# Kernel optimization log

Hardware: AMD Instinct MI355X
Metric: run time of the kernel (lower is better)

Reference implementation:

```python
import jax, jax.numpy as jnp
import numpy as np

N = 100000   # nodes
E = 1600000  # edges (avg degree 16)
IN, H, OUT = 64, 128, 1


def setup_inputs() -> dict:
    key = jax.random.key(0)
    ks = jax.random.split(key, 12)
    s = 0.05
    return {
        "x": jax.random.normal(ks[0], (N, IN), jnp.float32),
        "edge_index": jax.random.randint(ks[1], (2, E), 0, N, dtype=jnp.int64),
        "Wl1": jax.random.normal(ks[2], (IN, H), jnp.float32) * s,
        "Wr1": jax.random.normal(ks[3], (IN, H), jnp.float32) * s,
        "b1": jnp.zeros((H,), jnp.float32),
        "ln_g": jnp.ones((H,), jnp.float32),
        "ln_b": jnp.zeros((H,), jnp.float32),
        "Wres": jax.random.normal(ks[4], (IN, H), jnp.float32) * s,
        "bres": jnp.zeros((H,), jnp.float32),
        "Wl2": jax.random.normal(ks[5], (H, H), jnp.float32) * s,
        "Wr2": jax.random.normal(ks[6], (H, H), jnp.float32) * s,
        "b2": jnp.zeros((H,), jnp.float32),
        "Wl3": jax.random.normal(ks[7], (H, H), jnp.float32) * s,
        "Wr3": jax.random.normal(ks[8], (H, H), jnp.float32) * s,
        "b3": jnp.zeros((H,), jnp.float32),
        "Wl4": jax.random.normal(ks[9], (H, OUT), jnp.float32) * s,
        "Wr4": jax.random.normal(ks[10], (H, OUT), jnp.float32) * s,
        "b4": jnp.zeros((OUT,), jnp.float32),
    }


def _sage(h, src, dst, deg_inv, Wl, Wr, b):
    # PyG SAGEConv, aggr='mean': lin_l(mean_{j in N(i)} h_j) + lin_r(h_i)
    agg = jax.ops.segment_sum(h[src], dst, num_segments=N) * deg_inv[:, None]
    return agg @ Wl + h @ Wr + b


def _layernorm(h, g, b, eps=1e-5):
    mu = jnp.mean(h, axis=-1, keepdims=True)
    var = jnp.mean((h - mu) ** 2, axis=-1, keepdims=True)
    return (h - mu) * jax.lax.rsqrt(var + eps) * g + b


def reference(x, edge_index, Wl1, Wr1, b1, ln_g, ln_b, Wres, bres,
              Wl2, Wr2, b2, Wl3, Wr3, b3, Wl4, Wr4, b4):
    src, dst = edge_index[0], edge_index[1]
    deg = jax.ops.segment_sum(jnp.ones((E,), jnp.float32), dst, num_segments=N)
    deg_inv = 1.0 / jnp.maximum(deg, 1.0)

    h = jax.nn.relu(_layernorm(_sage(x, src, dst, deg_inv, Wl1, Wr1, b1), ln_g, ln_b))
    h = h + x @ Wres + bres              # residual (in_channel != hidden_channel)
    h = jax.nn.relu(_sage(h, src, dst, deg_inv, Wl2, Wr2, b2))   # dropout: eval no-op
    h = jax.nn.relu(_sage(h, src, dst, deg_inv, Wl3, Wr3, b3))
    out = _sage(h, src, dst, deg_inv, Wl4, Wr4, b4)
    return out.squeeze(-1)
```

## Files before the change

### kernel.cpp

```cpp
#include <hip/hip_runtime.h>
#include <hip/hip_bf16.h>

#define N_NODES 100000
#define N_EDGES 1600000

#define NBKT 782
#define SCAT_BLOCKS 240
#define BKT_CHUNK 6667

#define SORT_BLOCKS 40
#define SORT_CHUNK 2500
#define BH2_N (NBKT * SCAT_BLOCKS)
#define BHB ((BH2_N + 1023) / 1024)
#define XBF_BLOCKS 6250

#define NSTRIPS 6250
#define GEMM_BLOCKS 782

typedef __attribute__((ext_vector_type(8))) short short8v;
typedef __attribute__((ext_vector_type(4))) float float4v;

__device__ __forceinline__ unsigned short f2bf(float f) {
    unsigned int u = __float_as_uint(f);
    u = (u + 0x7FFFu + ((u >> 16) & 1u)) >> 16;
    return (unsigned short)u;
}
__device__ __forceinline__ float bf2f(unsigned short b) {
    return __uint_as_float((unsigned int)b << 16);
}

typedef __attribute__((address_space(1))) const unsigned int gld_g_t;
typedef __attribute__((address_space(3))) unsigned int gld_l_t;
__device__ __forceinline__ void gld_lds16(const void* g, void* l) {
    __builtin_amdgcn_global_load_lds((gld_g_t*)g, (gld_l_t*)l, 16, 0, 0);
}

#define SWZ128(row, ksh) ((row) * 128 + ((ksh) ^ (((row) & 7) << 3)))
#define SWZ256(row, ksh) ((row) * 256 + ((ksh) ^ (((row) & 7) << 3)))

__global__ __launch_bounds__(256) void hist_xbf_kernel(const int* __restrict__ ei, int* __restrict__ bh2,
                                                       const float* __restrict__ x, unsigned short* __restrict__ xsrc) {
    __shared__ int h[NBKT];
    int tid = threadIdx.x;
    if (blockIdx.x < SCAT_BLOCKS) {
        for (int i = tid; i < NBKT; i += 256) h[i] = 0;
        __syncthreads();
        int start = blockIdx.x * BKT_CHUNK;
        int end = start + BKT_CHUNK; if (end > N_EDGES) end = N_EDGES;
        for (int i = start + tid; i < end; i += 256) {
            int d = ei[N_EDGES + i];
            atomicAdd(&h[d >> 7], 1);
        }
        __syncthreads();
        for (int i = tid; i < NBKT; i += 256) bh2[i * SCAT_BLOCKS + blockIdx.x] = h[i];
    } else {
        int idx = (blockIdx.x - SCAT_BLOCKS) * 256 + tid;
        if (idx < N_NODES * 16) {
            int node = idx >> 4;
            int f0 = (idx & 15) * 4;
            float4 v = *(const float4*)(x + (size_t)idx * 4);
            ushort4 o;
            o.x = f2bf(v.x); o.y = f2bf(v.y); o.z = f2bf(v.z); o.w = f2bf(v.w);
            *(ushort4*)(xsrc + (size_t)node * 64 + f0) = o;
        }
    }
}

__global__ __launch_bounds__(256) void gscan_a_kernel(const int* __restrict__ in, int* __restrict__ bsum, int n) {
    __shared__ int lds[256];
    int tid = threadIdx.x;
    int base = blockIdx.x * 1024 + tid * 4;
    int s = 0;
    #pragma unroll
    for (int i = 0; i < 4; i++) s += (base + i < n) ? in[base + i] : 0;
    lds[tid] = s;
    __syncthreads();
    for (int off = 128; off; off >>= 1) {
        if (tid < off) lds[tid] += lds[tid + off];
        __syncthreads();
    }
    if (tid == 0) bsum[blockIdx.x] = lds[0];
}

__global__ __launch_bounds__(256) void gscan_c_kernel(int* __restrict__ data, const int* __restrict__ bsum,
                                                      int nb, int n) {
    __shared__ int sb[256];
    __shared__ int lds[256];
    int tid = threadIdx.x;
    sb[tid] = (tid < nb) ? bsum[tid] : 0;
    __syncthreads();
    for (int off = 1; off < 256; off <<= 1) {
        int y = 0;
        if (tid >= off) y = sb[tid - off];
        __syncthreads();
        if (tid >= off) sb[tid] += y;
        __syncthreads();
    }
    int blockbase = (blockIdx.x == 0) ? 0 : sb[blockIdx.x - 1];

    int base = blockIdx.x * 1024 + tid * 4;
    int v[4];
    int s = 0;
    #pragma unroll
    for (int i = 0; i < 4; i++) {
        v[i] = (base + i < n) ? data[base + i] : 0;
        s += v[i];
    }
    lds[tid] = s;
    __syncthreads();
    for (int off = 1; off < 256; off <<= 1) {
        int y = 0;
        if (tid >= off) y = lds[tid - off];
        __syncthreads();
        if (tid >= off) lds[tid] += y;
        __syncthreads();
    }
    int run = blockbase + lds[tid] - s;
    #pragma unroll
    for (int i = 0; i < 4; i++) {
        if (base + i < n) data[base + i] = run;
        run += v[i];
    }
}

__global__ __launch_bounds__(256) void bkt_scatter2_kernel(const int* __restrict__ ei, const int* __restrict__ bh2,
                                                           int* __restrict__ packed) {
    __shared__ int h[NBKT];
    __shared__ int base[NBKT];
    int tid = threadIdx.x;
    for (int i = tid; i < NBKT; i += 256) { h[i] = 0; base[i] = bh2[i * SCAT_BLOCKS + blockIdx.x]; }
    __syncthreads();
    int start = blockIdx.x * BKT_CHUNK;
    int end = start + BKT_CHUNK; if (end > N_EDGES) end = N_EDGES;
    for (int i = start + tid; i < end; i += 256) {
        int s = ei[i];
        int d = ei[N_EDGES + i];
        int b = d >> 7;
        int pos = base[b] + atomicAdd(&h[b], 1);
        packed[pos] = (s << 7) | (d & 127);
    }
}

__global__ __launch_bounds__(256) void bkt_build_kernel(const int* __restrict__ packed, const int* __restrict__ bh2,
                                                        int* __restrict__ deg, int* __restrict__ row_ptr,
                                                        int* __restrict__ col) {
    __shared__ int c[128];
    __shared__ int rp[128];
    int tid = threadIdx.x;
    int s0 = bh2[blockIdx.x * SCAT_BLOCKS];
    int s1 = (blockIdx.x + 1 < NBKT) ? bh2[(blockIdx.x + 1) * SCAT_BLOCKS] : N_EDGES;
    if (tid < 128) c[tid] = 0;
    __syncthreads();
    for (int i = s0 + tid; i < s1; i += 256) atomicAdd(&c[packed[i] & 127], 1);
    __syncthreads();
    if (tid < 128) rp[tid] = c[tid];
    __syncthreads();
    for (int off = 1; off < 128; off <<= 1) {
        int y = 0;
        if (tid >= off && tid < 128) y = rp[tid - off];
        __syncthreads();
        if (tid >= off && tid < 128) rp[tid] += y;
        __syncthreads();
    }
    int node = blockIdx.x * 128 + tid;
    if (tid < 128) {
        rp[tid] = s0 + rp[tid] - c[tid];
        if (node < N_NODES) {
            deg[node] = c[tid];
            row_ptr[node] = rp[tid];
        }
        c[tid] = 0;
    }
    if (blockIdx.x == 0 && tid == 0) row_ptr[N_NODES] = N_EDGES;
    __syncthreads();
    for (int i = s0 + tid; i < s1; i += 256) {
        int p = packed[i];
        int dl = p & 127;
        int pos = rp[dl] + atomicAdd(&c[dl], 1);
        col[pos] = p >> 7;
    }
}

__global__ __launch_bounds__(256) void dsort_hist_kernel(const int* __restrict__ deg, int* __restrict__ bh) {
    __shared__ int h[64];
    int tid = threadIdx.x;
    if (tid < 64) h[tid] = 0;
    __syncthreads();
    int start = blockIdx.x * SORT_CHUNK;
    int end = start + SORT_CHUNK; if (end > N_NODES) end = N_NODES;
    for (int i = start + tid; i < end; i += 256) atomicAdd(&h[63 - min(deg[i], 63)], 1);
    __syncthreads();
    if (tid < 64) bh[tid * SORT_BLOCKS + blockIdx.x] = h[tid];
}

__global__ __launch_bounds__(256) void dsort_scat_kernel(const int* __restrict__ deg, const int* __restrict__ bh,
                                                         int* __restrict__ ord) {
    __shared__ int sbh[64 * SORT_BLOCKS];
    __shared__ int ps[256];
    __shared__ int h[64];
    int tid = threadIdx.x;
    int v[10];
    int s = 0;
    #pragma unroll
    for (int k = 0; k < 10; k++) { v[k] = bh[tid * 10 + k]; s += v[k]; }
    ps[tid] = s;
    if (tid < 64) h[tid] = 0;
    __syncthreads();
    for (int off = 1; off < 256; off <<= 1) {
        int y = 0;
        if (tid >= off) y = ps[tid - off];
        __syncthreads();
        if (tid >= off) ps[tid] += y;
        __syncthreads();
    }
    int run = ps[tid] - s;
    #pragma unroll
    for (int k = 0; k < 10; k++) { sbh[tid * 10 + k] = run; run += v[k]; }
    __syncthreads();
    int start = blockIdx.x * SORT_CHUNK;
    int end = start + SORT_CHUNK; if (end > N_NODES) end = N_NODES;
    for (int i = start + tid; i < end; i += 256) {
        int b = 63 - min(deg[i], 63);
        int pos = sbh[b * SORT_BLOCKS + blockIdx.x] + atomicAdd(&h[b], 1);
        ord[pos] = i;
    }
}

#define ACC4(u) { a0 += bf2f(u.x); a1 += bf2f(u.y); a2 += bf2f(u.z); a3 += bf2f(u.w); }

__global__ __launch_bounds__(256) void agg64_kernel(const unsigned short* __restrict__ xsrc,
                                                    unsigned short* __restrict__ aggx,
                                                    const int* __restrict__ row_ptr, const int* __restrict__ col,
                                                    const int* __restrict__ ord) {
    int tid = threadIdx.x;
    int slot = blockIdx.x * 16 + (tid >> 4);
    if (slot >= N_NODES) return;
    int i = ord[slot];
    int f0 = (tid & 15) * 4;
    int s = row_ptr[i], e = row_ptr[i + 1];
    float a0 = 0.f, a1 = 0.f, a2 = 0.f, a3 = 0.f;
    int t = s;
    while (t + 7 < e) {
        int j0 = col[t], j1 = col[t + 1], j2 = col[t + 2], j3 = col[t + 3];
        int j4 = col[t + 4], j5 = col[t + 5], j6 = col[t + 6], j7 = col[t + 7];
        ushort4 u0 = *(const ushort4*)(xsrc + (size_t)j0 * 64 + f0);
        ushort4 u1 = *(const ushort4*)(xsrc + (size_t)j1 * 64 + f0);
        ushort4 u2 = *(const ushort4*)(xsrc + (size_t)j2 * 64 + f0);
        ushort4 u3 = *(const ushort4*)(xsrc + (size_t)j3 * 64 + f0);
        ushort4 u4 = *(const ushort4*)(xsrc + (size_t)j4 * 64 + f0);
        ushort4 u5 = *(const ushort4*)(xsrc + (size_t)j5 * 64 + f0);
        ushort4 u6 = *(const ushort4*)(xsrc + (size_t)j6 * 64 + f0);
        ushort4 u7 = *(const ushort4*)(xsrc + (size_t)j7 * 64 + f0);
        ACC4(u0) ACC4(u1) ACC4(u2) ACC4(u3) ACC4(u4) ACC4(u5) ACC4(u6) ACC4(u7)
        t += 8;
    }
    if (t + 3 < e) {
        int j0 = col[t], j1 = col[t + 1], j2 = col[t + 2], j3 = col[t + 3];
        ushort4 u0 = *(const ushort4*)(xsrc + (size_t)j0 * 64 + f0);
        ushort4 u1 = *(const ushort4*)(xsrc + (size_t)j1 * 64 + f0);
        ushort4 u2 = *(const ushort4*)(xsrc + (size_t)j2 * 64 + f0);
        ushort4 u3 = *(const ushort4*)(xsrc + (size_t)j3 * 64 + f0);
        ACC4(u0) ACC4(u1) ACC4(u2) ACC4(u3)
        t += 4;
    }
    if (t + 1 < e) {
        int j0 = col[t], j1 = col[t + 1];
        ushort4 u0 = *(const ushort4*)(xsrc + (size_t)j0 * 64 + f0);
        ushort4 u1 = *(const ushort4*)(xsrc + (size_t)j1 * 64 + f0);
        ACC4(u0) ACC4(u1)
        t += 2;
    }
    if (t < e) {
        ushort4 u0 = *(const ushort4*)(xsrc + (size_t)col[t] * 64 + f0);
        ACC4(u0)
    }
    float di = 1.0f / fmaxf((float)(e - s), 1.0f);
    ushort4 o;
    o.x = f2bf(a0 * di); o.y = f2bf(a1 * di); o.z = f2bf(a2 * di); o.w = f2bf(a3 * di);
    *(ushort4*)(aggx + (size_t)i * 64 + f0) = o;
}

__global__ __launch_bounds__(256) void agg128_kernel(const unsigned short* __restrict__ hsrc,
                                                     unsigned short* __restrict__ aggh,
                                                     const int* __restrict__ row_ptr, const int* __restrict__ col,
                                                     const int* __restrict__ ord) {
    int tid = threadIdx.x;
    int slot = blockIdx.x * 8 + (tid >> 5);
    if (slot >= N_NODES) return;
    int i = ord[slot];
    int f0 = (tid & 31) * 4;
    int s = row_ptr[i], e = row_ptr[i + 1];
    float a0 = 0.f, a1 = 0.f, a2 = 0.f, a3 = 0.f;
    int t = s;
    while (t + 7 < e) {
        int j0 = col[t], j1 = col[t + 1], j2 = col[t + 2], j3 = col[t + 3];
        int j4 = col[t + 4], j5 = col[t + 5], j6 = col[t + 6], j7 = col[t + 7];
        ushort4 u0 = *(const ushort4*)(hsrc + (size_t)j0 * 128 + f0);
        ushort4 u1 = *(const ushort4*)(hsrc + (size_t)j1 * 128 + f0);
        ushort4 u2 = *(const ushort4*)(hsrc + (size_t)j2 * 128 + f0);
        ushort4 u3 = *(const ushort4*)(hsrc + (size_t)j3 * 128 + f0);
        ushort4 u4 = *(const ushort4*)(hsrc + (size_t)j4 * 128 + f0);
        ushort4 u5 = *(const ushort4*)(hsrc + (size_t)j5 * 128 + f0);
        ushort4 u6 = *(const ushort4*)(hsrc + (size_t)j6 * 128 + f0);
        ushort4 u7 = *(const ushort4*)(hsrc + (size_t)j7 * 128 + f0);
        ACC4(u0) ACC4(u1) ACC4(u2) ACC4(u3) ACC4(u4) ACC4(u5) ACC4(u6) ACC4(u7)
        t += 8;
    }
    if (t + 3 < e) {
        int j0 = col[t], j1 = col[t + 1], j2 = col[t + 2], j3 = col[t + 3];
        ushort4 u0 = *(const ushort4*)(hsrc + (size_t)j0 * 128 + f0);
        ushort4 u1 = *(const ushort4*)(hsrc + (size_t)j1 * 128 + f0);
        ushort4 u2 = *(const ushort4*)(hsrc + (size_t)j2 * 128 + f0);
        ushort4 u3 = *(const ushort4*)(hsrc + (size_t)j3 * 128 + f0);
        ACC4(u0) ACC4(u1) ACC4(u2) ACC4(u3)
        t += 4;
    }
    if (t + 1 < e) {
        int j0 = col[t], j1 = col[t + 1];
        ushort4 u0 = *(const ushort4*)(hsrc + (size_t)j0 * 128 + f0);
        ushort4 u1 = *(const ushort4*)(hsrc + (size_t)j1 * 128 + f0);
        ACC4(u0) ACC4(u1)
        t += 2;
    }
    if (t < e) {
        ushort4 u0 = *(const ushort4*)(hsrc + (size_t)col[t] * 128 + f0);
        ACC4(u0)
    }
    float di = 1.0f / fmaxf((float)(e - s), 1.0f);
    ushort4 o;
    o.x = f2bf(a0 * di); o.y = f2bf(a1 * di); o.z = f2bf(a2 * di); o.w = f2bf(a3 * di);
    *(ushort4*)(aggh + (size_t)i * 128 + f0) = o;
}

__global__ __launch_bounds__(256) void wprep_all_kernel(const float* __restrict__ Wr1, const float* __restrict__ Wl1,
                                                        const float* __restrict__ Wres,
                                                        const float* __restrict__ Wl2, const float* __restrict__ Wr2,
                                                        const float* __restrict__ Wl3, const float* __restrict__ Wr3,
                                                        unsigned short* __restrict__ Bt1,
                                                        unsigned short* __restrict__ Bt2,
                                                        unsigned short* __restrict__ Bt3) {
    int idx = blockIdx.x * 256 + threadIdx.x;
    int seg = idx >> 15;
    int loc = idx & 32767;
    if (seg == 0) {
        int n = loc >> 7;
        int k = loc & 127;
        float v;
        if (n < 128) v = (k < 64) ? Wr1[k * 128 + n] : Wl1[(k - 64) * 128 + n];
        else         v = (k < 64) ? Wres[k * 128 + (n - 128)] : 0.f;
        Bt1[loc] = f2bf(v);
    } else if (seg == 1) {
        int n = loc >> 8;
        int k = loc & 255;
        float v = (k < 128) ? Wr2[k * 128 + n] : Wl2[(k - 128) * 128 + n];
        Bt2[loc] = f2bf(v);
    } else if (seg == 2) {
        int n = loc >> 8;
        int k = loc & 255;
        float v = (k < 128) ? Wr3[k * 128 + n] : Wl3[(k - 128) * 128 + n];
        Bt3[loc] = f2bf(v);
    }
}

__global__ __launch_bounds__(512) void mgemm1_ln_kernel(const unsigned short* __restrict__ Ax,
                                                        const unsigned short* __restrict__ Aa,
                                                        const unsigned short* __restrict__ Bt,
                                                        const float* __restrict__ b1, const float* __restrict__ ln_g,
                                                        const float* __restrict__ ln_b, const float* __restrict__ bres,
                                                        unsigned short* __restrict__ hsrc) {
    __shared__ unsigned short Bs[32768];
    int tid = threadIdx.x;
    int wave = tid >> 6, lane = tid & 63;
    int lm = lane & 15, lk = (lane >> 4) * 8;

    #pragma unroll
    for (int rnd = 0; rnd < 8; rnd++) {
        int Lb = rnd * 8192 + tid * 16;
        int row = Lb >> 8;
        int sb = (Lb & 255) ^ ((row & 7) << 4);
        gld_lds16(Bt + (size_t)row * 128 + (sb >> 1), &Bs[Lb >> 1]);
    }
    __syncthreads();

    int strip = blockIdx.x * 8 + wave;
    if (strip >= NSTRIPS) return;
    int m0 = strip * 16;

    float4v accT[8], accR[8];
    #pragma unroll
    for (int j = 0; j < 8; j++) { accT[j] = (float4v)0.f; accR[j] = (float4v)0.f; }

    const unsigned short* arx = Ax + (size_t)(m0 + lm) * 64 + lk;
    const unsigned short* ara = Aa + (size_t)(m0 + lm) * 64 + lk;
    #pragma unroll
    for (int k0 = 0; k0 < 128; k0 += 32) {
        short8v af = (k0 < 64) ? *(const short8v*)(arx + k0) : *(const short8v*)(ara + (k0 - 64));
        short8v bf[8];
        #pragma unroll
        for (int j = 0; j < 8; j++)
            bf[j] = *(const short8v*)&Bs[SWZ128(j * 16 + lm, k0 + lk)];
        #pragma unroll
        for (int j = 0; j < 8; j++)
            accT[j] = __builtin_amdgcn_mfma_f32_16x16x32_bf16(af, bf[j], accT[j], 0, 0, 0);
        if (k0 < 64) {
            short8v bg[8];
            #pragma unroll
            for (int j = 0; j < 8; j++)
                bg[j] = *(const short8v*)&Bs[SWZ128(128 + j * 16 + lm, k0 + lk)];
            #pragma unroll
            for (int j = 0; j < 8; j++)
                accR[j] = __builtin_amdgcn_mfma_f32_16x16x32_bf16(af, bg[j], accR[j], 0, 0, 0);
        }
    }

    float b1v[8], gv[8], bbv[8], brv[8];
    #pragma unroll
    for (int j = 0; j < 8; j++) {
        int cc = j * 16 + lm;
        b1v[j] = b1[cc]; gv[j] = ln_g[cc]; bbv[j] = ln_b[cc]; brv[j] = bres[cc];
    }
    int q4 = lane >> 4;
    #pragma unroll
    for (int r = 0; r < 4; r++) {
        float sp = 0.f, sq = 0.f;
        #pragma unroll
        for (int j = 0; j < 8; j++) {
            float tv = accT[j][r] + b1v[j];
            sp += tv; sq += tv * tv;
        }
        #pragma unroll
        for (int off = 1; off < 16; off <<= 1) {
            sp += __shfl_xor(sp, off);
            sq += __shfl_xor(sq, off);
        }
        float mu = sp * (1.f / 128.f);
        float var = sq * (1.f / 128.f) - mu * mu;
        float rstd = rsqrtf(var + 1e-5f);
        int gm = m0 + q4 * 4 + r;
        #pragma unroll
        for (int j = 0; j < 8; j++) {
            float tv = accT[j][r] + b1v[j];
            float y = fmaxf((tv - mu) * rstd * gv[j] + bbv[j], 0.f) + accR[j][r] + brv[j];
            hsrc[(size_t)gm * 128 + j * 16 + lm] = f2bf(y);
        }
    }
}

__global__ __launch_bounds__(512) void mgemm_kernel(const unsigned short* __restrict__ Ah,
                                                    const unsigned short* __restrict__ Aa,
                                                    const unsigned short* __restrict__ Bt,
                                                    const float* __restrict__ bias,
                                                    unsigned short* __restrict__ C) {
    __shared__ unsigned short Bs[32768];
    int tid = threadIdx.x;
    int wave = tid >> 6, lane = tid & 63;
    int lm = lane & 15, lk = (lane >> 4) * 8;

    #pragma unroll
    for (int rnd = 0; rnd < 8; rnd++) {
        int Lb = rnd * 8192 + tid * 16;
        int row = Lb >> 9;
        int sb = (Lb & 511) ^ ((row & 7) << 4);
        gld_lds16(Bt + ((size_t)row << 8) + (sb >> 1), &Bs[Lb >> 1]);
    }
    __syncthreads();

    int strip = blockIdx.x * 8 + wave;
    if (strip >= NSTRIPS) return;
    int m0 = strip * 16;

    float4v acc[8];
    #pragma unroll
    for (int j = 0; j < 8; j++) acc[j] = (float4v)0.f;

    const unsigned short* arh = Ah + (size_t)(m0 + lm) * 128 + lk;
    const unsigned short* ara = Aa + (size_t)(m0 + lm) * 128 + lk;
    #pragma unroll
    for (int k0 = 0; k0 < 256; k0 += 32) {
        short8v af = (k0 < 128) ? *(const short8v*)(arh + k0) : *(const short8v*)(ara + (k0 - 128));
        short8v bf[8];
        #pragma unroll
        for (int j = 0; j < 8; j++)
            bf[j] = *(const short8v*)&Bs[SWZ256(j * 16 + lm, k0 + lk)];
        #pragma unroll
        for (int j = 0; j < 8; j++)
            acc[j] = __builtin_amdgcn_mfma_f32_16x16x32_bf16(af, bf[j], acc[j], 0, 0, 0);
    }

    int q4 = lane >> 4;
    #pragma unroll
    for (int j = 0; j < 8; j++) {
        int cc = j * 16 + lm;
        float bv = bias[cc];
        #pragma unroll
        for (int r = 0; r < 4; r++) {
            int m = m0 + q4 * 4 + r;
            C[(size_t)m * 128 + cc] = f2bf(fmaxf(acc[j][r] + bv, 0.f));
        }
    }
}

__global__ __launch_bounds__(512) void mgemm_pq_kernel(const unsigned short* __restrict__ Ah,
                                                       const unsigned short* __restrict__ Aa,
                                                       const unsigned short* __restrict__ Bt,
                                                       const float* __restrict__ bias,
                                                       const float* __restrict__ Wl4, const float* __restrict__ Wr4,
                                                       const float* __restrict__ b4,
                                                       float* __restrict__ p, float* __restrict__ q) {
    __shared__ unsigned short Bs[32768];
    int tid = threadIdx.x;
    int wave = tid >> 6, lane = tid & 63;
    int lm = lane & 15, lk = (lane >> 4) * 8;

    #pragma unroll
    for (int rnd = 0; rnd < 8; rnd++) {
        int Lb = rnd * 8192 + tid * 16;
        int row = Lb >> 9;
        int sb = (Lb & 511) ^ ((row & 7) << 4);
        gld_lds16(Bt + ((size_t)row << 8) + (sb >> 1), &Bs[Lb >> 1]);
    }
    __syncthreads();

    int strip = blockIdx.x * 8 + wave;
    if (strip >= NSTRIPS) return;
    int m0 = strip * 16;

    float4v acc[8];
    #pragma unroll
    for (int j = 0; j < 8; j++) acc[j] = (float4v)0.f;

    const unsigned short* arh = Ah + (size_t)(m0 + lm) * 128 + lk;
    const unsigned short* ara = Aa + (size_t)(m0 + lm) * 128 + lk;
    #pragma unroll
    for (int k0 = 0; k0 < 256; k0 += 32) {
        short8v af = (k0 < 128) ? *(const short8v*)(arh + k0) : *(const short8v*)(ara + (k0 - 128));
        short8v bf[8];
        #pragma unroll
        for (int j = 0; j < 8; j++)
            bf[j] = *(const short8v*)&Bs[SWZ256(j * 16 + lm, k0 + lk)];
        #pragma unroll
        for (int j = 0; j < 8; j++)
            acc[j] = __builtin_amdgcn_mfma_f32_16x16x32_bf16(af, bf[j], acc[j], 0, 0, 0);
    }

    float b3v[8], wlv[8], wrv[8];
    #pragma unroll
    for (int j = 0; j < 8; j++) {
        int cc = j * 16 + lm;
        b3v[j] = bias[cc]; wlv[j] = Wl4[cc]; wrv[j] = Wr4[cc];
    }
    float b4v = b4[0];
    int q4 = lane >> 4;
    #pragma unroll
    for (int r = 0; r < 4; r++) {
        float pp = 0.f, qq = 0.f;
        #pragma unroll
        for (int j = 0; j < 8; j++) {
            float hv = fmaxf(acc[j][r] + b3v[j], 0.f);
            pp += hv * wlv[j]; qq += hv * wrv[j];
        }
        #pragma unroll
        for (int off = 1; off < 16; off <<= 1) {
            pp += __shfl_xor(pp, off);
            qq += __shfl_xor(qq, off);
        }
        if (lm == 0) {
            int m = m0 + q4 * 4 + r;
            p[m] = pp;
            q[m] = qq + b4v;
        }
    }
}

__global__ __launch_bounds__(256) void final_kernel(const float* __restrict__ p, const float* __restrict__ q,
                                                    const int* __restrict__ row_ptr, const int* __restrict__ col,
                                                    float* __restrict__ out) {
    int i = blockIdx.x * 256 + threadIdx.x;
    if (i >= N_NODES) return;
    int s = row_ptr[i], e = row_ptr[i + 1];
    float acc = 0.f;
    int t = s;
    for (; t + 7 < e; t += 8)
        acc += p[col[t]] + p[col[t + 1]] + p[col[t + 2]] + p[col[t + 3]]
             + p[col[t + 4]] + p[col[t + 5]] + p[col[t + 6]] + p[col[t + 7]];
    for (; t < e; t++) acc += p[col[t]];
    float di = 1.0f / fmaxf((float)(e - s), 1.0f);
    out[i] = acc * di + q[i];
}


extern "C" void kernel_launch(void* const* d_in, const int* in_sizes, int n_in,
                              void* d_out, int out_size, void* d_ws, size_t ws_size,
                              hipStream_t stream) {
    const float* x    = (const float*)d_in[0];
    const int*   ei   = (const int*)d_in[1];
    const float* Wl1  = (const float*)d_in[2];
    const float* Wr1  = (const float*)d_in[3];
    const float* b1   = (const float*)d_in[4];
    const float* ln_g = (const float*)d_in[5];
    const float* ln_b = (const float*)d_in[6];
    const float* Wres = (const float*)d_in[7];
    const float* bres = (const float*)d_in[8];
    const float* Wl2  = (const float*)d_in[9];
    const float* Wr2  = (const float*)d_in[10];
    const float* b2   = (const float*)d_in[11];
    const float* Wl3  = (const float*)d_in[12];
    const float* Wr3  = (const float*)d_in[13];
    const float* b3   = (const float*)d_in[14];
    const float* Wl4  = (const float*)d_in[15];
    const float* Wr4  = (const float*)d_in[16];
    const float* b4   = (const float*)d_in[17];
    float* out = (float*)d_out;

    char* w = (char*)d_ws;
    size_t off = 0;
    auto alloc = [&](size_t bytes) -> void* {
        off = (off + 255) & ~(size_t)255;
        void* pp = w + off;
        off += bytes;
        return pp;
    };

    int*   deg        = (int*)alloc(N_NODES * 4);
    int*   row_ptr    = (int*)alloc((N_NODES + 1) * 4);
    int*   bsum       = (int*)alloc(1024);
    int*   col        = (int*)alloc(N_EDGES * 4);
    int*   bh2        = (int*)alloc(BH2_N * 4);
    int*   bh         = (int*)alloc(64 * SORT_BLOCKS * 4);
    int*   ord        = (int*)alloc(N_NODES * 4);
    unsigned short* Bt1  = (unsigned short*)alloc(256 * 128 * 2);
    unsigned short* Bt2  = (unsigned short*)alloc(128 * 256 * 2);
    unsigned short* Bt3  = (unsigned short*)alloc(128 * 256 * 2);
    unsigned short* xsrc = (unsigned short*)alloc((size_t)N_NODES * 64 * 2);
    unsigned short* aggx = (unsigned short*)alloc((size_t)N_NODES * 64 * 2);
    unsigned short* hsrc = (unsigned short*)alloc((size_t)N_NODES * 128 * 2);
    unsigned short* aggh = (unsigned short*)alloc((size_t)N_NODES * 128 * 2);
    int*   packed  = (int*)alloc((size_t)N_EDGES * 4);
    float* p       = (float*)alloc(N_NODES * 4);
    float* q       = (float*)alloc(N_NODES * 4);
    (void)ws_size; (void)n_in; (void)in_sizes; (void)out_size;

    const int NB = (N_NODES + 255) / 256;

    wprep_all_kernel<<<384, 256, 0, stream>>>(Wr1, Wl1, Wres, Wl2, Wr2, Wl3, Wr3, Bt1, Bt2, Bt3);

    hist_xbf_kernel<<<SCAT_BLOCKS + XBF_BLOCKS, 256, 0, stream>>>(ei, bh2, x, xsrc);
    gscan_a_kernel<<<BHB, 256, 0, stream>>>(bh2, bsum, BH2_N);
    gscan_c_kernel<<<BHB, 256, 0, stream>>>(bh2, bsum, BHB, BH2_N);
    bkt_scatter2_kernel<<<SCAT_BLOCKS, 256, 0, stream>>>(ei, bh2, packed);
    bkt_build_kernel<<<NBKT, 256, 0, stream>>>(packed, bh2, deg, row_ptr, col);
    dsort_hist_kernel<<<SORT_BLOCKS, 256, 0, stream>>>(deg, bh);
    dsort_scat_kernel<<<SORT_BLOCKS, 256, 0, stream>>>(deg, bh, ord);

    agg64_kernel<<<(N_NODES + 15) / 16, 256, 0, stream>>>(xsrc, aggx, row_ptr, col, ord);
    mgemm1_ln_kernel<<<GEMM_BLOCKS, 512, 0, stream>>>(xsrc, aggx, Bt1, b1, ln_g, ln_b, bres, hsrc);

    agg128_kernel<<<(N_NODES + 7) / 8, 256, 0, stream>>>(hsrc, aggh, row_ptr, col, ord);
    mgemm_kernel<<<GEMM_BLOCKS, 512, 0, stream>>>(hsrc, aggh, Bt2, b2, hsrc);

    agg128_kernel<<<(N_NODES + 7) / 8, 256, 0, stream>>>(hsrc, aggh, row_ptr, col, ord);
    mgemm_pq_kernel<<<GEMM_BLOCKS, 512, 0, stream>>>(hsrc, aggh, Bt3, b3, Wl4, Wr4, b4, p, q);

    final_kernel<<<NB, 256, 0, stream>>>(p, q, row_ptr, col, out);
}
```

Measured before the change: 368.2 us.

## Merge CSR build preprocessing kernels and use global-atomic bucket scatter

Folds weight prep, the destination-bucket histogram and the x-to-bf16 conversion into one launch, and replaces the per-block histogram plus two-pass global scan with a global atomic bucket histogram scanned by a single 1024-thread block. The bucket scatter now uses global atomic counters with twice as many blocks, and the degree-sort histogram is computed inside the CSR build kernel, removing the separate dsort_hist pass. The aim is fewer launches and less scan traffic, at the cost of global atomic contention on 782 counters, an extra memset, and a nondeterministic edge order within each bucket.

After: 793.8 us. 116% more time.

```diff
diff --git a/kernel.cpp b/kernel.cpp
--- a/kernel.cpp
+++ b/kernel.cpp
@@ -5,14 +5,17 @@
 #define N_EDGES 1600000
 
 #define NBKT 782
-#define SCAT_BLOCKS 240
-#define BKT_CHUNK 6667
+
+#define WPREP_BLOCKS 384
+#define HIST_BLOCKS 240
+#define HIST_CHUNK 6667
+#define XBF_BLOCKS 6250
+
+#define SCATB 480
+#define SCHUNK 3334
 
 #define SORT_BLOCKS 40
 #define SORT_CHUNK 2500
-#define BH2_N (NBKT * SCAT_BLOCKS)
-#define BHB ((BH2_N + 1023) / 1024)
-#define XBF_BLOCKS 6250
 
 #define NSTRIPS 6250
 #define GEMM_BLOCKS 782
@@ -38,23 +41,54 @@
 #define SWZ128(row, ksh) ((row) * 128 + ((ksh) ^ (((row) & 7) << 3)))
 #define SWZ256(row, ksh) ((row) * 256 + ((ksh) ^ (((row) & 7) << 3)))
 
-__global__ __launch_bounds__(256) void hist_xbf_kernel(const int* __restrict__ ei, int* __restrict__ bh2,
-                                                       const float* __restrict__ x, unsigned short* __restrict__ xsrc) {
+__global__ __launch_bounds__(256) void mega0_kernel(const float* __restrict__ Wr1, const float* __restrict__ Wl1,
+                                                    const float* __restrict__ Wres,
+                                                    const float* __restrict__ Wl2, const float* __restrict__ Wr2,
+                                                    const float* __restrict__ Wl3, const float* __restrict__ Wr3,
+                                                    unsigned short* __restrict__ Bt1,
+                                                    unsigned short* __restrict__ Bt2,
+                                                    unsigned short* __restrict__ Bt3,
+                                                    const int* __restrict__ ei, int* __restrict__ csr_hist,
+                                                    const float* __restrict__ x, unsigned short* __restrict__ xsrc) {
     __shared__ int h[NBKT];
     int tid = threadIdx.x;
-    if (blockIdx.x < SCAT_BLOCKS) {
+    int bid = blockIdx.x;
+    if (bid < WPREP_BLOCKS) {
+        int idx = bid * 256 + tid;
+        int seg = idx >> 15;
+        int loc = idx & 32767;
+        if (seg == 0) {
+            int n = loc >> 7;
+            int k = loc & 127;
+            float v;
+            if (n < 128) v = (k < 64) ? Wr1[k * 128 + n] : Wl1[(k - 64) * 128 + n];
+            else         v = (k < 64) ? Wres[k * 128 + (n - 128)] : 0.f;
+            Bt1[loc] = f2bf(v);
+        } else if (seg == 1) {
+            int n = loc >> 8;
+            int k = loc & 255;
+            float v = (k < 128) ? Wr2[k * 128 + n] : Wl2[(k - 128) * 128 + n];
+            Bt2[loc] = f2bf(v);
+        } else {
+            int n = loc >> 8;
+            int k = loc & 255;
+            float v = (k < 128) ? Wr3[k * 128 + n] : Wl3[(k - 128) * 128 + n];
+            Bt3[loc] = f2bf(v);
+        }
+    } else if (bid < WPREP_BLOCKS + HIST_BLOCKS) {
         for (int i = tid; i < NBKT; i += 256) h[i] = 0;
         __syncthreads();
-        int start = blockIdx.x * BKT_CHUNK;
-        int end = start + BKT_CHUNK; if (end > N_EDGES) end = N_EDGES;
+        int start = (bid - WPREP_BLOCKS) * HIST_CHUNK;
+        int end = start + HIST_CHUNK; if (end > N_EDGES) end = N_EDGES;
         for (int i = start + tid; i < end; i += 256) {
             int d = ei[N_EDGES + i];
             atomicAdd(&h[d >> 7], 1);
         }
         __syncthreads();
-        for (int i = tid; i < NBKT; i += 256) bh2[i * SCAT_BLOCKS + blockIdx.x] = h[i];
+        for (int i = tid; i < NBKT; i += 256)
+            if (h[i]) atomicAdd(&csr_hist[i], h[i]);
     } else {
-        int idx = (blockIdx.x - SCAT_BLOCKS) * 256 + tid;
+        int idx = (bid - WPREP_BLOCKS - HIST_BLOCKS) * 256 + tid;
         if (idx < N_NODES * 16) {
             int node = idx >> 4;
             int f0 = (idx & 15) * 4;
@@ -66,89 +100,45 @@
     }
 }
 
-__global__ __launch_bounds__(256) void gscan_a_kernel(const int* __restrict__ in, int* __restrict__ bsum, int n) {
-    __shared__ int lds[256];
-    int tid = threadIdx.x;
-    int base = blockIdx.x * 1024 + tid * 4;
-    int s = 0;
-    #pragma unroll
-    for (int i = 0; i < 4; i++) s += (base + i < n) ? in[base + i] : 0;
-    lds[tid] = s;
-    __syncthreads();
-    for (int off = 128; off; off >>= 1) {
-        if (tid < off) lds[tid] += lds[tid + off];
-        __syncthreads();
-    }
-    if (tid == 0) bsum[blockIdx.x] = lds[0];
-}
-
-__global__ __launch_bounds__(256) void gscan_c_kernel(int* __restrict__ data, const int* __restrict__ bsum,
-                                                      int nb, int n) {
-    __shared__ int sb[256];
-    __shared__ int lds[256];
-    int tid = threadIdx.x;
-    sb[tid] = (tid < nb) ? bsum[tid] : 0;
-    __syncthreads();
-    for (int off = 1; off < 256; off <<= 1) {
-        int y = 0;
-        if (tid >= off) y = sb[tid - off];
-        __syncthreads();
-        if (tid >= off) sb[tid] += y;
-        __syncthreads();
-    }
-    int blockbase = (blockIdx.x == 0) ? 0 : sb[blockIdx.x - 1];
-
-    int base = blockIdx.x * 1024 + tid * 4;
-    int v[4];
-    int s = 0;
-    #pragma unroll
-    for (int i = 0; i < 4; i++) {
-        v[i] = (base + i < n) ? data[base + i] : 0;
-        s += v[i];
-    }
-    lds[tid] = s;
-    __syncthreads();
-    for (int off = 1; off < 256; off <<= 1) {
+__global__ __launch_bounds__(1024) void scan782_kernel(const int* __restrict__ hist, int* __restrict__ base) {
+    __shared__ int lds[1024];
+    int tid = threadIdx.x;
+    int v = (tid < NBKT) ? hist[tid] : 0;
+    lds[tid] = v;
+    __syncthreads();
+    for (int off = 1; off < 1024; off <<= 1) {
         int y = 0;
         if (tid >= off) y = lds[tid - off];
         __syncthreads();
         if (tid >= off) lds[tid] += y;
         __syncthreads();
     }
-    int run = blockbase + lds[tid] - s;
-    #pragma unroll
-    for (int i = 0; i < 4; i++) {
-        if (base + i < n) data[base + i] = run;
-        run += v[i];
-    }
-}
-
-__global__ __launch_bounds__(256) void bkt_scatter2_kernel(const int* __restrict__ ei, const int* __restrict__ bh2,
-                                                           int* __restrict__ packed) {
-    __shared__ int h[NBKT];
-    __shared__ int base[NBKT];
-    int tid = threadIdx.x;
-    for (int i = tid; i < NBKT; i += 256) { h[i] = 0; base[i] = bh2[i * SCAT_BLOCKS + blockIdx.x]; }
-    __syncthreads();
-    int start = blockIdx.x * BKT_CHUNK;
-    int end = start + BKT_CHUNK; if (end > N_EDGES) end = N_EDGES;
+    if (tid < NBKT) base[tid] = lds[tid] - v;
+    if (tid == 0) base[NBKT] = N_EDGES;
+}
+
+__global__ __launch_bounds__(256) void bscat_kernel(const int* __restrict__ ei, const int* __restrict__ base,
+                                                    int* __restrict__ cnt, int* __restrict__ packed) {
+    int tid = threadIdx.x;
+    int start = blockIdx.x * SCHUNK;
+    int end = start + SCHUNK; if (end > N_EDGES) end = N_EDGES;
     for (int i = start + tid; i < end; i += 256) {
         int s = ei[i];
         int d = ei[N_EDGES + i];
         int b = d >> 7;
-        int pos = base[b] + atomicAdd(&h[b], 1);
+        int pos = base[b] + atomicAdd(&cnt[b], 1);
         packed[pos] = (s << 7) | (d & 127);
     }
 }
 
-__global__ __launch_bounds__(256) void bkt_build_kernel(const int* __restrict__ packed, const int* __restrict__ bh2,
+__global__ __launch_bounds__(256) void bkt_build_kernel(const int* __restrict__ packed, const int* __restrict__ base,
                                                         int* __restrict__ deg, int* __restrict__ row_ptr,
-                                                        int* __restrict__ col) {
+                                                        int* __restrict__ col, int* __restrict__ dbh) {
     __shared__ int c[128];
     __shared__ int rp[128];
     int tid = threadIdx.x;
-    int s0 = bh2[blockIdx.x * SCAT_BLOCKS];
-    int s1 = (blockIdx.x + 1 < NBKT) ? bh2[(blockIdx.x + 1) * SCAT_BLOCKS] : N_EDGES;
+    int s0 = base[blockIdx.x];
+    int s1 = base[blockIdx.x + 1];
     if (tid < 128) c[tid] = 0;
     __syncthreads();
     for (int i = s0 + tid; i < s1; i += 256) atomicAdd(&c[packed[i] & 127], 1);
@@ -168,6 +158,8 @@
         if (node < N_NODES) {
             deg[node] = c[tid];
             row_ptr[node] = rp[tid];
+            int b = 63 - min(c[tid], 63);
+            atomicAdd(&dbh[b * SORT_BLOCKS + node / SORT_CHUNK], 1);
         }
         c[tid] = 0;
     }
@@ -179,18 +171,6 @@
         int pos = rp[dl] + atomicAdd(&c[dl], 1);
         col[pos] = p >> 7;
     }
-}
-
-__global__ __launch_bounds__(256) void dsort_hist_kernel(const int* __restrict__ deg, int* __restrict__ bh) {
-    __shared__ int h[64];
-    int tid = threadIdx.x;
-    if (tid < 64) h[tid] = 0;
-    __syncthreads();
-    int start = blockIdx.x * SORT_CHUNK;
-    int end = start + SORT_CHUNK; if (end > N_NODES) end = N_NODES;
-    for (int i = start + tid; i < end; i += 256) atomicAdd(&h[63 - min(deg[i], 63)], 1);
-    __syncthreads();
-    if (tid < 64) bh[tid * SORT_BLOCKS + blockIdx.x] = h[tid];
 }
 
 __global__ __launch_bounds__(256) void dsort_scat_kernel(const int* __restrict__ deg, const int* __restrict__ bh,
@@ -330,36 +310,6 @@
     ushort4 o;
     o.x = f2bf(a0 * di); o.y = f2bf(a1 * di); o.z = f2bf(a2 * di); o.w = f2bf(a3 * di);
     *(ushort4*)(aggh + (size_t)i * 128 + f0) = o;
-}
-
-__global__ __launch_bounds__(256) void wprep_all_kernel(const float* __restrict__ Wr1, const float* __restrict__ Wl1,
-                                                        const float* __restrict__ Wres,
-                                                        const float* __restrict__ Wl2, const float* __restrict__ Wr2,
-                                                        const float* __restrict__ Wl3, const float* __restrict__ Wr3,
-                                                        unsigned short* __restrict__ Bt1,
-                                                        unsigned short* __restrict__ Bt2,
-                                                        unsigned short* __restrict__ Bt3) {
-    int idx = blockIdx.x * 256 + threadIdx.x;
-    int seg = idx >> 15;
-    int loc = idx & 32767;
-    if (seg == 0) {
-        int n = loc >> 7;
-        int k = loc & 127;
-        float v;
-        if (n < 128) v = (k < 64) ? Wr1[k * 128 + n] : Wl1[(k - 64) * 128 + n];
-        else         v = (k < 64) ? Wres[k * 128 + (n - 128)] : 0.f;
-        Bt1[loc] = f2bf(v);
-    } else if (seg == 1) {
-        int n = loc >> 8;
-        int k = loc & 255;
-        float v = (k < 128) ? Wr2[k * 128 + n] : Wl2[(k - 128) * 128 + n];
-        Bt2[loc] = f2bf(v);
-    } else if (seg == 2) {
-        int n = loc >> 8;
-        int k = loc & 255;
-        float v = (k < 128) ? Wr3[k * 128 + n] : Wl3[(k - 128) * 128 + n];
-        Bt3[loc] = f2bf(v);
-    }
 }
 
 __global__ __launch_bounds__(512) void mgemm1_ln_kernel(const unsigned short* __restrict__ Ax,
@@ -621,13 +571,15 @@
         return pp;
     };
 
-    int*   deg        = (int*)alloc(N_NODES * 4);
-    int*   row_ptr    = (int*)alloc((N_NODES + 1) * 4);
-    int*   bsum       = (int*)alloc(1024);
-    int*   col        = (int*)alloc(N_EDGES * 4);
-    int*   bh2        = (int*)alloc(BH2_N * 4);
-    int*   bh         = (int*)alloc(64 * SORT_BLOCKS * 4);
-    int*   ord        = (int*)alloc(N_NODES * 4);
+    int* meta     = (int*)alloc((NBKT + NBKT + 64 * SORT_BLOCKS) * 4);
+    int* csr_hist = meta;
+    int* csr_cnt  = meta + NBKT;
+    int* dbh      = meta + 2 * NBKT;
+    int* base     = (int*)alloc((NBKT + 1) * 4);
+    int* deg      = (int*)alloc(N_NODES * 4);
+    int* row_ptr  = (int*)alloc((N_NODES + 1) * 4);
+    int* col      = (int*)alloc(N_EDGES * 4);
+    int* ord      = (int*)alloc(N_NODES * 4);
     unsigned short* Bt1  = (unsigned short*)alloc(256 * 128 * 2);
     unsigned short* Bt2  = (unsigned short*)alloc(128 * 256 * 2);
     unsigned short* Bt3  = (unsigned short*)alloc(128 * 256 * 2);
@@ -642,15 +594,14 @@
 
     const int NB = (N_NODES + 255) / 256;
 
-    wprep_all_kernel<<<384, 256, 0, stream>>>(Wr1, Wl1, Wres, Wl2, Wr2, Wl3, Wr3, Bt1, Bt2, Bt3);
-
-    hist_xbf_kernel<<<SCAT_BLOCKS + XBF_BLOCKS, 256, 0, stream>>>(ei, bh2, x, xsrc);
-    gscan_a_kernel<<<BHB, 256, 0, stream>>>(bh2, bsum, BH2_N);
-    gscan_c_kernel<<<BHB, 256, 0, stream>>>(bh2, bsum, BHB, BH2_N);
-    bkt_scatter2_kernel<<<SCAT_BLOCKS, 256, 0, stream>>>(ei, bh2, packed);
-    bkt_build_kernel<<<NBKT, 256, 0, stream>>>(packed, bh2, deg, row_ptr, col);
-    dsort_hist_kernel<<<SORT_BLOCKS, 256, 0, stream>>>(deg, bh);
-    dsort_scat_kernel<<<SORT_BLOCKS, 256, 0, stream>>>(deg, bh, ord);
+    hipMemsetAsync(meta, 0, (NBKT + NBKT + 64 * SORT_BLOCKS) * 4, stream);
+    mega0_kernel<<<WPREP_BLOCKS + HIST_BLOCKS + XBF_BLOCKS, 256, 0, stream>>>(
+        Wr1, Wl1, Wres, Wl2, Wr2, Wl3, Wr3, Bt1, Bt2, Bt3, ei, csr_hist, x, xsrc);
+
+    scan782_kernel<<<1, 1024, 0, stream>>>(csr_hist, base);
+    bscat_kernel<<<SCATB, 256, 0, stream>>>(ei, base, csr_cnt, packed);
+    bkt_build_kernel<<<NBKT, 256, 0, stream>>>(packed, base, deg, row_ptr, col, dbh);
+    dsort_scat_kernel<<<SORT_BLOCKS, 256, 0, stream>>>(deg, dbh, ord);
 
     agg64_kernel<<<(N_NODES + 15) / 16, 256, 0, stream>>>(xsrc, aggx, row_ptr, col, ord);
     mgemm1_ln_kernel<<<GEMM_BLOCKS, 512, 0, stream>>>(xsrc, aggx, Bt1, b1, ln_g, ln_b, bres, hsrc);
```
